# Kernel tuning notes

Hardware: AMD Instinct MI355X
Metric: run time of the kernel (lower is better)

## Reference

```python
import jax, jax.numpy as jnp
import numpy as np

N_NODES = 50000
N_EDGES = 800000
D_FEAT = 128


def setup_inputs() -> dict:
    key = jax.random.key(0)
    k1, k2, k3, k4, k5, k6 = jax.random.split(key, 6)
    input = jax.random.normal(k1, (N_NODES, D_FEAT), dtype=jnp.float32)
    h0 = jax.random.normal(k2, (N_NODES, D_FEAT), dtype=jnp.float32)
    # edge list + weights represent the sparse normalized adjacency used by torch.spmm
    edge_row = jax.random.randint(k3, (N_EDGES,), 0, N_NODES, dtype=jnp.int32)
    edge_col = jax.random.randint(k4, (N_EDGES,), 0, N_NODES, dtype=jnp.int32)
    edge_weight = jax.random.uniform(k5, (N_EDGES,), dtype=jnp.float32)
    # learned parameter: uniform(-stdv, stdv) with stdv = 1/sqrt(out_features)
    stdv = 1.0 / np.sqrt(D_FEAT)
    weight = jax.random.uniform(k6, (D_FEAT, D_FEAT), dtype=jnp.float32,
                                minval=-stdv, maxval=stdv)
    return {
        "input": input,
        "h0": h0,
        "weight": weight,
        "edge_row": edge_row,
        "edge_col": edge_col,
        "edge_weight": edge_weight,
        "lamda": jnp.float32(0.5),
        "alpha": jnp.float32(0.1),
        "l": 4,
    }


def reference(input, h0, weight, edge_row, edge_col, edge_weight, lamda, alpha, l):
    n = input.shape[0]
    # theta = min(1, log(lamda / l + 1))
    theta = jnp.minimum(jnp.float32(1.0), jnp.log(lamda / l + 1.0))
    # hi = spmm(adj, input): gather source features, scale by edge weight, scatter-add to dest rows
    hi = jax.ops.segment_sum(edge_weight[:, None] * input[edge_col], edge_row,
                             num_segments=n)  # [N, D]
    support = (1.0 - alpha) * hi + alpha * h0
    output = theta * (support @ weight) + (1.0 - theta) * support
    return output + input
```

## Files before the change

### kernel.cpp

```cpp
#include <hip/hip_runtime.h>
#include <hip/hip_fp16.h>

#define D_FEAT 128

typedef _Float16 half8_t __attribute__((ext_vector_type(8)));
typedef float float4_t __attribute__((ext_vector_type(4)));

__device__ __forceinline__ float h16_to_f(unsigned short u) {
    union { unsigned short u; _Float16 f; } cv; cv.u = u; return (float)cv.f;
}
__device__ __forceinline__ unsigned short f_to_h16(float f) {
    union { unsigned short u; _Float16 f; } cv; cv.f = (_Float16)f; return cv.u;
}

__global__ __launch_bounds__(256) void prep_kernel(
    const float* __restrict__ input, unsigned* __restrict__ inph_u2,
    const float* __restrict__ W, __half* __restrict__ wt16,
    unsigned* __restrict__ sedge4_slack,
    const int* __restrict__ erow, int* __restrict__ bucket_cnt,
    int nconv4, int n_edges, int convBlocks, int wBlocks)
{
    __shared__ int lh[256];
    const int bid = blockIdx.x;
    const int t = threadIdx.x;

    if (bid < convBlocks) {
        int tid = bid * 256 + t;
        if (tid < nconv4) {
            float4 v = reinterpret_cast<const float4*>(input)[tid];
            __half2 a = __floats2half2_rn(v.x, v.y);
            __half2 b = __floats2half2_rn(v.z, v.w);
            uint2 p;
            p.x = *reinterpret_cast<unsigned*>(&a);
            p.y = *reinterpret_cast<unsigned*>(&b);
            reinterpret_cast<uint2*>(inph_u2)[tid] = p;
        }
    } else if (bid < convBlocks + wBlocks) {
        int idx = (bid - convBlocks) * 256 + t;
        if (idx < D_FEAT * D_FEAT) {
            int n = idx >> 7, k = idx & 127;
            wt16[n * D_FEAT + k] = __float2half(W[k * D_FEAT + n]);
        }
    } else if (bid == convBlocks + wBlocks) {
        if (t < 16) sedge4_slack[t] = 0u;
    } else {
        int hb = bid - convBlocks - wBlocks - 1;
        lh[t] = 0;
        __syncthreads();
        int base = hb * 4096;
        int end = base + 4096; if (end > n_edges) end = n_edges;
        for (int i = base + t; i < end; i += 256)
            atomicAdd(&lh[erow[i] >> 8], 1);
        __syncthreads();
        int c = lh[t];
        if (c > 0) atomicAdd(&bucket_cnt[t], c);
    }
}

__global__ __launch_bounds__(256) void bucket_scan_kernel(
    const int* __restrict__ bucket_cnt, int* __restrict__ bcursor,
    int* __restrict__ bbase, int nb, int n_edges)
{
    __shared__ int lds[256];
    int t = threadIdx.x;
    int v = (t < nb) ? bucket_cnt[t] : 0;
    lds[t] = v;
    __syncthreads();
#pragma unroll
    for (int off = 1; off < 256; off <<= 1) {
        int add = (t >= off) ? lds[t - off] : 0;
        __syncthreads();
        lds[t] += add;
        __syncthreads();
    }
    if (t < nb) {
        int ex = lds[t] - v;
        bcursor[t] = ex;
        bbase[t] = ex;
    }
    if (t == 0) bbase[nb] = n_edges;
}

__global__ __launch_bounds__(256) void bin_kernel(
    const int* __restrict__ erow, const int* __restrict__ ecol,
    const float* __restrict__ ew, int* __restrict__ bcursor,
    uint2* __restrict__ btmp, int n_edges)
{
    __shared__ int lcnt[256];
    const int t = threadIdx.x;
    const int base = blockIdx.x * 4096;
    lcnt[t] = 0;
    __syncthreads();

    unsigned rc[16];
    float    wv[16];
#pragma unroll
    for (int i = 0; i < 16; ++i) {
        int idx = base + i * 256 + t;
        if (idx < n_edges) {
            int r = erow[idx];
            rc[i] = ((unsigned)r << 16) | (unsigned)ecol[idx];
            wv[i] = ew[idx];
            atomicAdd(&lcnt[r >> 8], 1);
        } else {
            rc[i] = 0xFFFFFFFFu;
        }
    }
    __syncthreads();
    int c = lcnt[t];
    int gbase = (c > 0) ? atomicAdd(&bcursor[t], c) : 0;
    lcnt[t] = gbase;
    __syncthreads();
#pragma unroll
    for (int i = 0; i < 16; ++i) {
        if (rc[i] != 0xFFFFFFFFu) {
            int b = rc[i] >> 24;
            int pos = atomicAdd(&lcnt[b], 1);
            uint2 p;
            p.x = rc[i];
            p.y = __float_as_uint(wv[i]);
            btmp[pos] = p;
        }
    }
}

__global__ __launch_bounds__(256) void sort_kernel(
    const uint2* __restrict__ btmp, const int* __restrict__ bbase,
    int* __restrict__ cnt, int* __restrict__ beg,
    unsigned* __restrict__ sedge4, int n)
{
    __shared__ int lscan[256];
    __shared__ int lofs[256];
    const int b = blockIdx.x;
    const int t = threadIdx.x;
    const int lo = bbase[b];
    const int hi = bbase[b + 1];

    lscan[t] = 0;
    __syncthreads();
    for (int i = lo + t; i < hi; i += 256) {
        int rl = (btmp[i].x >> 16) & 255;
        atomicAdd(&lscan[rl], 1);
    }
    __syncthreads();
    int v = lscan[t];
    __syncthreads();
#pragma unroll
    for (int off = 1; off < 256; off <<= 1) {
        int add = (t >= off) ? lscan[t - off] : 0;
        __syncthreads();
        lscan[t] += add;
        __syncthreads();
    }
    int ex = lscan[t] - v;
    lofs[t] = ex;
    int row = b * 256 + t;
    if (row < n) {
        cnt[row] = v;
        beg[row] = lo + ex;
    }
    __syncthreads();
    for (int i = lo + t; i < hi; i += 256) {
        uint2 p = btmp[i];
        int rl = (p.x >> 16) & 255;
        int pos = atomicAdd(&lofs[rl], 1);
        float w = __uint_as_float(p.y);
        sedge4[lo + pos] = (p.x & 0xFFFFu) | ((unsigned)f_to_h16(w) << 16);
    }
}

__global__ __launch_bounds__(256) void spmm4_kernel(
    const __half2* __restrict__ inph, const float* __restrict__ h0,
    const int* __restrict__ begp, const int* __restrict__ cnt,
    const unsigned* __restrict__ sedge4,
    const float* __restrict__ alpha_p, __half2* __restrict__ s16out, int n)
{
    int lane = threadIdx.x & 63;
    int row  = blockIdx.x * 4 + (threadIdx.x >> 6);
    if (row >= n) return;

    int deg = cnt[row];
    int beg = begp[row];

    float2 a0 = {0.f, 0.f}, a1 = {0.f, 0.f}, a2 = {0.f, 0.f}, a3 = {0.f, 0.f};
    for (int e = 0; e < deg; e += 16) {
        unsigned r[16];
#pragma unroll
        for (int i = 0; i < 16; ++i) r[i] = sedge4[beg + e + i];
        __half2 v[16];
#pragma unroll
        for (int i = 0; i < 16; ++i)
            v[i] = inph[(size_t)(r[i] & 0xFFFFu) * 64 + lane];
#pragma unroll
        for (int i = 0; i < 16; ++i) {
            float w = h16_to_f((e + i < deg) ? (unsigned short)(r[i] >> 16)
                                             : (unsigned short)0);
            float2 f = __half22float2(v[i]);
            if ((i & 3) == 0) { a0.x = fmaf(w, f.x, a0.x); a0.y = fmaf(w, f.y, a0.y); }
            if ((i & 3) == 1) { a1.x = fmaf(w, f.x, a1.x); a1.y = fmaf(w, f.y, a1.y); }
            if ((i & 3) == 2) { a2.x = fmaf(w, f.x, a2.x); a2.y = fmaf(w, f.y, a2.y); }
            if ((i & 3) == 3) { a3.x = fmaf(w, f.x, a3.x); a3.y = fmaf(w, f.y, a3.y); }
        }
    }
    float2 acc;
    acc.x = (a0.x + a1.x) + (a2.x + a3.x);
    acc.y = (a0.y + a1.y) + (a2.y + a3.y);

    const float alpha = alpha_p[0];
    const float oma   = 1.0f - alpha;
    float2 h = reinterpret_cast<const float2*>(h0)[(size_t)row * 64 + lane];
    float sx = fmaf(oma, acc.x, alpha * h.x);
    float sy = fmaf(oma, acc.y, alpha * h.y);
    s16out[(size_t)row * 64 + lane] = __floats2half2_rn(sx, sy);
}

__global__ __launch_bounds__(256) void gemm_mfma_kernel(
    const __half* __restrict__ s16, const __half* __restrict__ wt16,
    const float* __restrict__ input, float* __restrict__ out,
    const float* __restrict__ lamda_p, const int* __restrict__ l_p,
    int n_rows)
{
    const int wave = threadIdx.x >> 6;
    const int lane = threadIdx.x & 63;
    const int row0 = (blockIdx.x * 4 + wave) * 16;
    if (row0 >= n_rows) return;

    const int mr = lane & 15;
    const int kg = lane >> 4;

    const _Float16* sp = reinterpret_cast<const _Float16*>(s16);
    const _Float16* wp = reinterpret_cast<const _Float16*>(wt16);

    float4_t acc[8];
#pragma unroll
    for (int nt = 0; nt < 8; ++nt) acc[nt] = (float4_t){0.f, 0.f, 0.f, 0.f};

#pragma unroll
    for (int ks = 0; ks < 4; ++ks) {
        const int kofs = ks * 32 + kg * 8;
        half8_t a = *reinterpret_cast<const half8_t*>(
            sp + (size_t)(row0 + mr) * D_FEAT + kofs);
#pragma unroll
        for (int nt = 0; nt < 8; ++nt) {
            half8_t b = *reinterpret_cast<const half8_t*>(
                wp + (size_t)(nt * 16 + mr) * D_FEAT + kofs);
            acc[nt] = __builtin_amdgcn_mfma_f32_16x16x32_f16(a, b, acc[nt], 0, 0, 0);
        }
    }

    const float lamda = lamda_p[0];
    const float theta = fminf(1.0f, logf(lamda / (float)l_p[0] + 1.0f));
    const float om_theta = 1.0f - theta;

#pragma unroll
    for (int nt = 0; nt < 8; ++nt) {
#pragma unroll
        for (int r = 0; r < 4; ++r) {
            const int row = row0 + kg * 4 + r;
            const int col = nt * 16 + mr;
            const size_t idx = (size_t)row * D_FEAT + col;
            const float s = (float)sp[idx];
            out[idx] = fmaf(theta, acc[nt][r], fmaf(om_theta, s, input[idx]));
        }
    }
}

__global__ __launch_bounds__(256) void hist_kernel(
    const int* __restrict__ erow, int* __restrict__ cnt, int n_edges)
{
    int e = blockIdx.x * 256 + threadIdx.x;
    if (e < n_edges) atomicAdd(&cnt[erow[e]], 1);
}

__global__ __launch_bounds__(256) void prep_noW_kernel(
    const float* __restrict__ input, unsigned* __restrict__ inph_u2,
    const int* __restrict__ erow, int* __restrict__ cnt,
    int nconv4, int n_edges)
{
    int tid = blockIdx.x * 256 + threadIdx.x;
    if (tid < nconv4) {
        float4 v = reinterpret_cast<const float4*>(input)[tid];
        __half2 a = __floats2half2_rn(v.x, v.y);
        __half2 b = __floats2half2_rn(v.z, v.w);
        uint2 p;
        p.x = *reinterpret_cast<unsigned*>(&a);
        p.y = *reinterpret_cast<unsigned*>(&b);
        reinterpret_cast<uint2*>(inph_u2)[tid] = p;
    } else {
        int e = tid - nconv4;
        if (e < n_edges) atomicAdd(&cnt[erow[e]], 1);
    }
}

__global__ __launch_bounds__(256) void partial_kernel(
    const int* __restrict__ cnt, int* __restrict__ partial, int n)
{
    __shared__ int lds[4];
    int i = blockIdx.x * 256 + threadIdx.x;
    int v = (i < n) ? cnt[i] : 0;
#pragma unroll
    for (int off = 32; off > 0; off >>= 1) v += __shfl_down(v, off, 64);
    if ((threadIdx.x & 63) == 0) lds[threadIdx.x >> 6] = v;
    __syncthreads();
    if (threadIdx.x == 0)
        partial[blockIdx.x] = lds[0] + lds[1] + lds[2] + lds[3];
}

__global__ __launch_bounds__(256) void scan_partial_kernel(
    int* __restrict__ partial, int nb)
{
    __shared__ int lds[256];
    int t = threadIdx.x;
    int v = (t < nb) ? partial[t] : 0;
    lds[t] = v;
    __syncthreads();
#pragma unroll
    for (int off = 1; off < 256; off <<= 1) {
        int add = (t >= off) ? lds[t - off] : 0;
        __syncthreads();
        lds[t] += add;
        __syncthreads();
    }
    if (t < nb) partial[t] = lds[t] - v;
}

__global__ __launch_bounds__(256) void scan_final_kernel(
    const int* __restrict__ cnt, const int* __restrict__ partial,
    int* __restrict__ cursor, int n)
{
    __shared__ int lds[256];
    int t = threadIdx.x;
    int i = blockIdx.x * 256 + t;
    int v = (i < n) ? cnt[i] : 0;
    lds[t] = v;
    __syncthreads();
#pragma unroll
    for (int off = 1; off < 256; off <<= 1) {
        int add = (t >= off) ? lds[t - off] : 0;
        __syncthreads();
        lds[t] += add;
        __syncthreads();
    }
    if (i < n) cursor[i] = lds[t] - v + partial[blockIdx.x];
}

__global__ __launch_bounds__(256) void edge_scatter_kernel(
    const int* __restrict__ erow, const int* __restrict__ ecol,
    const float* __restrict__ ew, int* __restrict__ cursor,
    uint2* __restrict__ sedge, int n_edges)
{
    int e = blockIdx.x * 256 + threadIdx.x;
    if (e >= n_edges) return;
    int r = erow[e];
    int pos = atomicAdd(&cursor[r], 1);
    uint2 p;
    p.x = (unsigned)ecol[e];
    p.y = __float_as_uint(ew[e]);
    sedge[pos] = p;
}

__global__ __launch_bounds__(256) void spmm_fp16_kernel(
    const __half2* __restrict__ inph, const float* __restrict__ h0,
    const int* __restrict__ cursor, const int* __restrict__ cnt,
    const uint2* __restrict__ sedge,
    const float* __restrict__ alpha_p, float* __restrict__ outp, int n)
{
    int lane = threadIdx.x & 63;
    int row  = blockIdx.x * 4 + (threadIdx.x >> 6);
    if (row >= n) return;
    int deg = cnt[row];
    int beg = cursor[row] - deg;
    float2 accA = make_float2(0.f, 0.f), accB = make_float2(0.f, 0.f);
    int e = 0;
    for (; e + 2 <= deg; e += 2) {
        uint2 e0 = sedge[beg + e], e1 = sedge[beg + e + 1];
        __half2 v0 = inph[(size_t)e0.x * 64 + lane];
        __half2 v1 = inph[(size_t)e1.x * 64 + lane];
        float w0 = __uint_as_float(e0.y), w1 = __uint_as_float(e1.y);
        float2 f0 = __half22float2(v0), f1 = __half22float2(v1);
        accA.x = fmaf(w0, f0.x, accA.x); accA.y = fmaf(w0, f0.y, accA.y);
        accB.x = fmaf(w1, f1.x, accB.x); accB.y = fmaf(w1, f1.y, accB.y);
    }
    if (e < deg) {
        uint2 e0 = sedge[beg + e];
        __half2 v0 = inph[(size_t)e0.x * 64 + lane];
        float w0 = __uint_as_float(e0.y);
        float2 f0 = __half22float2(v0);
        accA.x = fmaf(w0, f0.x, accA.x); accA.y = fmaf(w0, f0.y, accA.y);
    }
    float2 acc; acc.x = accA.x + accB.x; acc.y = accA.y + accB.y;
    const float alpha = alpha_p[0], oma = 1.0f - alpha;
    float2 h = reinterpret_cast<const float2*>(h0)[(size_t)row * 64 + lane];
    float2 s;
    s.x = fmaf(oma, acc.x, alpha * h.x);
    s.y = fmaf(oma, acc.y, alpha * h.y);
    reinterpret_cast<float2*>(outp)[(size_t)row * 64 + lane] = s;
}

__global__ __launch_bounds__(256) void spmm_fp32_kernel(
    const float* __restrict__ input, const float* __restrict__ h0,
    const int* __restrict__ cursor, const int* __restrict__ cnt,
    const uint2* __restrict__ sedge,
    const float* __restrict__ alpha_p, float* __restrict__ outp, int n)
{
    int lane = threadIdx.x & 63;
    int row  = blockIdx.x * 4 + (threadIdx.x >> 6);
    if (row >= n) return;
    int deg = cnt[row];
    int beg = cursor[row] - deg;
    const float2* in2 = reinterpret_cast<const float2*>(input);
    float2 acc = make_float2(0.f, 0.f);
    for (int e = 0; e < deg; ++e) {
        uint2 ed = sedge[beg + e];
        float w = __uint_as_float(ed.y);
        float2 v = in2[(size_t)ed.x * 64 + lane];
        acc.x = fmaf(w, v.x, acc.x);
        acc.y = fmaf(w, v.y, acc.y);
    }
    const float alpha = alpha_p[0], oma = 1.0f - alpha;
    float2 h = reinterpret_cast<const float2*>(h0)[(size_t)row * 64 + lane];
    float2 s;
    s.x = fmaf(oma, acc.x, alpha * h.x);
    s.y = fmaf(oma, acc.y, alpha * h.y);
    reinterpret_cast<float2*>(outp)[(size_t)row * 64 + lane] = s;
}

__global__ __launch_bounds__(256) void fused_kernel(
    float* __restrict__ io, const float* __restrict__ input,
    const float* __restrict__ W,
    const float* __restrict__ lamda_p, const int* __restrict__ l_p,
    int n_rows)
{
    __shared__ float s_lds[2][D_FEAT];
    const int j = threadIdx.x & 127;
    const int r = threadIdx.x >> 7;
    float wcol[D_FEAT];
#pragma unroll
    for (int k = 0; k < D_FEAT; ++k) wcol[k] = W[k * D_FEAT + j];
    const float lamda = lamda_p[0];
    const float theta = fminf(1.0f, logf(lamda / (float)l_p[0] + 1.0f));
    const float om_theta = 1.0f - theta;
    for (int row0 = blockIdx.x * 2; row0 < n_rows; row0 += gridDim.x * 2) {
        const int row = row0 + r;
        const bool active = row < n_rows;
        float sj = 0.0f;
        if (active) {
            sj = io[(size_t)row * D_FEAT + j];
            s_lds[r][j] = sj;
        }
        __syncthreads();
        if (active) {
            float dot = 0.0f;
            const float4* s4 = reinterpret_cast<const float4*>(s_lds[r]);
#pragma unroll
            for (int k4 = 0; k4 < D_FEAT / 4; ++k4) {
                const float4 sv = s4[k4];
                dot = fmaf(sv.x, wcol[4 * k4 + 0], dot);
                dot = fmaf(sv.y, wcol[4 * k4 + 1], dot);
                dot = fmaf(sv.z, wcol[4 * k4 + 2], dot);
                dot = fmaf(sv.w, wcol[4 * k4 + 3], dot);
            }
            const size_t base = (size_t)row * D_FEAT + j;
            io[base] = fmaf(theta, dot, om_theta * sj) + input[base];
        }
        __syncthreads();
    }
}

extern "C" void kernel_launch(void* const* d_in, const int* in_sizes, int n_in,
                              void* d_out, int out_size, void* d_ws, size_t ws_size,
                              hipStream_t stream)
{
    const float* input = (const float*)d_in[0];
    const float* h0    = (const float*)d_in[1];
    const float* W     = (const float*)d_in[2];
    const int*   erow  = (const int*)d_in[3];
    const int*   ecol  = (const int*)d_in[4];
    const float* ew    = (const float*)d_in[5];
    const float* lamda = (const float*)d_in[6];
    const float* alpha = (const float*)d_in[7];
    const int*   l_p   = (const int*)d_in[8];
    float* out = (float*)d_out;

    const int n_nodes = in_sizes[0] / D_FEAT;
    const int n_edges = in_sizes[3];
    const int nb = (n_nodes + 255) / 256;
    const int nconv4 = n_nodes * D_FEAT / 4;
    const int histBlocks = (n_edges + 4095) / 4096;

    char* p = (char*)d_ws;
    auto align16 = [](char* q) {
        return (char*)(((uintptr_t)q + 15) & ~(uintptr_t)15);
    };
    int* cnt      = (int*)p;                    p += (size_t)n_nodes * 4;
    int* beg      = (int*)p;                    p += (size_t)n_nodes * 4;
    int* bucket_cnt = (int*)p;                  p += 256 * 4;
    int* bcursor  = (int*)p;                    p += 257 * 4;
    int* bbase    = (int*)p;                    p += 257 * 4;
    p = align16(p);
    unsigned* sedge4 = (unsigned*)p;            p += ((size_t)n_edges + 16) * 4;
    p = align16(p);
    unsigned* inph  = (unsigned*)p;             p += (size_t)n_nodes * D_FEAT * 2;
    p = align16(p);
    char* unionp = p;
    uint2*  btmp = (uint2*)unionp;
    __half* s16  = (__half*)unionp;
    size_t union_bytes = (size_t)n_nodes * D_FEAT * 2;
    if ((size_t)n_edges * 8 > union_bytes) union_bytes = (size_t)n_edges * 8;
    p += union_bytes;
    p = align16(p);
    __half* wt16 = (__half*)p;                  p += (size_t)D_FEAT * D_FEAT * 2;
    const size_t need_new = (size_t)(p - (char*)d_ws);

    const bool use_new = (ws_size >= need_new) && (n_nodes < 65536) && (nb <= 256);

    if (use_new) {
        const int convBlocks = (nconv4 + 255) / 256;
        const int wBlocks = (D_FEAT * D_FEAT + 255) / 256;
        const int totalBlocks = convBlocks + wBlocks + 1 + histBlocks;

        hipMemsetAsync(bucket_cnt, 0, 256 * sizeof(int), stream);
        prep_kernel<<<totalBlocks, 256, 0, stream>>>(
            input, inph, W, wt16, sedge4 + n_edges, erow, bucket_cnt,
            nconv4, n_edges, convBlocks, wBlocks);
        bucket_scan_kernel<<<1, 256, 0, stream>>>(
            bucket_cnt, bcursor, bbase, nb, n_edges);
        bin_kernel<<<histBlocks, 256, 0, stream>>>(
            erow, ecol, ew, bcursor, btmp, n_edges);
        sort_kernel<<<nb, 256, 0, stream>>>(
            btmp, bbase, cnt, beg, sedge4, n_nodes);
        spmm4_kernel<<<(n_nodes + 3) / 4, 256, 0, stream>>>(
            (const __half2*)inph, h0, beg, cnt, sedge4, alpha,
            (__half2*)s16, n_nodes);
        const int ntiles = (n_nodes + 15) / 16;
        gemm_mfma_kernel<<<(ntiles + 3) / 4, 256, 0, stream>>>(
            s16, wt16, input, out, lamda, l_p, n_nodes);
        return;
    }

    int*   fcnt     = (int*)d_ws;
    int*   fcursor  = fcnt + n_nodes;
    int*   fpartial = fcursor + n_nodes;
    uint2* fsedge   = (uint2*)(fpartial + 256);
    unsigned* finph = (unsigned*)(fsedge + n_edges);

    const size_t need_base = (size_t)(2 * n_nodes + 256) * 4 + (size_t)n_edges * 8;
    const size_t need_fp16 = need_base + (size_t)n_nodes * D_FEAT * 2;
    const bool use_fp16 = ws_size >= need_fp16;

    hipMemsetAsync(fcnt, 0, (size_t)n_nodes * sizeof(int), stream);

    if (use_fp16) {
        int total = nconv4 + n_edges;
        prep_noW_kernel<<<(total + 255) / 256, 256, 0, stream>>>(
            input, finph, erow, fcnt, nconv4, n_edges);
    } else {
        hist_kernel<<<(n_edges + 255) / 256, 256, 0, stream>>>(erow, fcnt, n_edges);
    }
    partial_kernel<<<nb, 256, 0, stream>>>(fcnt, fpartial, n_nodes);
    scan_partial_kernel<<<1, 256, 0, stream>>>(fpartial, nb);
    scan_final_kernel<<<nb, 256, 0, stream>>>(fcnt, fpartial, fcursor, n_nodes);
    edge_scatter_kernel<<<(n_edges + 255) / 256, 256, 0, stream>>>(
        erow, ecol, ew, fcursor, fsedge, n_edges);
    if (use_fp16) {
        spmm_fp16_kernel<<<(n_nodes + 3) / 4, 256, 0, stream>>>(
            (const __half2*)finph, h0, fcursor, fcnt, fsedge, alpha, out, n_nodes);
    } else {
        spmm_fp32_kernel<<<(n_nodes + 3) / 4, 256, 0, stream>>>(
            input, h0, fcursor, fcnt, fsedge, alpha, out, n_nodes);
    }
    fused_kernel<<<2048, 256, 0, stream>>>(out, input, W, lamda, l_p, n_nodes);
}
```

Baseline: 118.1 us.

## Fuse bucket scan into prep via last-block ticket; split SpMM wave into half-waves

The separate single-block bucket scan kernel is removed. Its work now runs inside prep_kernel, in whichever histogram block is the last to finish, detected with a global done counter and a threadfence, which saves one kernel launch. The SpMM kernel is reorganised so each half-wave handles alternate edges and loads 8-byte chunks (4 halves) per lane, with a cross-half shuffle reduction at the end. This halves the gathers issued per lane per 16-edge chunk and widens each load, at the cost of a final shuffle and an idle half-wave during the epilogue store.

```diff
diff --git a/kernel.cpp b/kernel.cpp
--- a/kernel.cpp
+++ b/kernel.cpp
@@ -18,9 +18,13 @@
     const float* __restrict__ W, __half* __restrict__ wt16,
     unsigned* __restrict__ sedge4_slack,
     const int* __restrict__ erow, int* __restrict__ bucket_cnt,
-    int nconv4, int n_edges, int convBlocks, int wBlocks)
+    int* __restrict__ done_ctr, int* __restrict__ bcursor,
+    int* __restrict__ bbase,
+    int nconv4, int n_edges, int convBlocks, int wBlocks,
+    int histBlocks, int nb)
 {
     __shared__ int lh[256];
+    __shared__ int ticket_s;
     const int bid = blockIdx.x;
     const int t = threadIdx.x;
 
@@ -54,31 +58,29 @@
         __syncthreads();
         int c = lh[t];
         if (c > 0) atomicAdd(&bucket_cnt[t], c);
-    }
-}
-
-__global__ __launch_bounds__(256) void bucket_scan_kernel(
-    const int* __restrict__ bucket_cnt, int* __restrict__ bcursor,
-    int* __restrict__ bbase, int nb, int n_edges)
-{
-    __shared__ int lds[256];
-    int t = threadIdx.x;
-    int v = (t < nb) ? bucket_cnt[t] : 0;
-    lds[t] = v;
-    __syncthreads();
-#pragma unroll
-    for (int off = 1; off < 256; off <<= 1) {
-        int add = (t >= off) ? lds[t - off] : 0;
-        __syncthreads();
-        lds[t] += add;
-        __syncthreads();
-    }
-    if (t < nb) {
-        int ex = lds[t] - v;
-        bcursor[t] = ex;
-        bbase[t] = ex;
-    }
-    if (t == 0) bbase[nb] = n_edges;
+        __threadfence();
+        __syncthreads();
+        if (t == 0) ticket_s = atomicAdd(done_ctr, 1);
+        __syncthreads();
+        if (ticket_s == histBlocks - 1) {
+            int v = (t < nb) ? atomicAdd(&bucket_cnt[t], 0) : 0;
+            lh[t] = v;
+            __syncthreads();
+#pragma unroll
+            for (int off = 1; off < 256; off <<= 1) {
+                int add = (t >= off) ? lh[t - off] : 0;
+                __syncthreads();
+                lh[t] += add;
+                __syncthreads();
+            }
+            if (t < nb) {
+                int ex = lh[t] - v;
+                bcursor[t] = ex;
+                bbase[t] = ex;
+            }
+            if (t == 0) bbase[nb] = n_edges;
+        }
+    }
 }
 
 __global__ __launch_bounds__(256) void bin_kernel(
@@ -170,48 +172,90 @@
 }
 
 __global__ __launch_bounds__(256) void spmm4_kernel(
-    const __half2* __restrict__ inph, const float* __restrict__ h0,
+    const uint2* __restrict__ inph2, const float* __restrict__ h0,
     const int* __restrict__ begp, const int* __restrict__ cnt,
     const unsigned* __restrict__ sedge4,
-    const float* __restrict__ alpha_p, __half2* __restrict__ s16out, int n)
-{
-    int lane = threadIdx.x & 63;
-    int row  = blockIdx.x * 4 + (threadIdx.x >> 6);
+    const float* __restrict__ alpha_p, uint2* __restrict__ s16out, int n)
+{
+    const int lane = threadIdx.x & 63;
+    const int row  = blockIdx.x * 4 + (threadIdx.x >> 6);
     if (row >= n) return;
 
-    int deg = cnt[row];
-    int beg = begp[row];
-
-    float2 a0 = {0.f, 0.f}, a1 = {0.f, 0.f}, a2 = {0.f, 0.f}, a3 = {0.f, 0.f};
+    const int g  = lane >> 5;
+    const int fl = lane & 31;
+
+    const int deg = cnt[row];
+    const int beg = begp[row];
+
+    float4 accA = {0.f, 0.f, 0.f, 0.f};
+    float4 accB = {0.f, 0.f, 0.f, 0.f};
+
     for (int e = 0; e < deg; e += 16) {
-        unsigned r[16];
-#pragma unroll
-        for (int i = 0; i < 16; ++i) r[i] = sedge4[beg + e + i];
-        __half2 v[16];
-#pragma unroll
-        for (int i = 0; i < 16; ++i)
-            v[i] = inph[(size_t)(r[i] & 0xFFFFu) * 64 + lane];
-#pragma unroll
-        for (int i = 0; i < 16; ++i) {
-            float w = h16_to_f((e + i < deg) ? (unsigned short)(r[i] >> 16)
-                                             : (unsigned short)0);
-            float2 f = __half22float2(v[i]);
-            if ((i & 3) == 0) { a0.x = fmaf(w, f.x, a0.x); a0.y = fmaf(w, f.y, a0.y); }
-            if ((i & 3) == 1) { a1.x = fmaf(w, f.x, a1.x); a1.y = fmaf(w, f.y, a1.y); }
-            if ((i & 3) == 2) { a2.x = fmaf(w, f.x, a2.x); a2.y = fmaf(w, f.y, a2.y); }
-            if ((i & 3) == 3) { a3.x = fmaf(w, f.x, a3.x); a3.y = fmaf(w, f.y, a3.y); }
-        }
-    }
-    float2 acc;
-    acc.x = (a0.x + a1.x) + (a2.x + a3.x);
-    acc.y = (a0.y + a1.y) + (a2.y + a3.y);
-
-    const float alpha = alpha_p[0];
-    const float oma   = 1.0f - alpha;
-    float2 h = reinterpret_cast<const float2*>(h0)[(size_t)row * 64 + lane];
-    float sx = fmaf(oma, acc.x, alpha * h.x);
-    float sy = fmaf(oma, acc.y, alpha * h.y);
-    s16out[(size_t)row * 64 + lane] = __floats2half2_rn(sx, sy);
+        unsigned r0 = sedge4[beg + e +  0 + g];
+        unsigned r1 = sedge4[beg + e +  2 + g];
+        unsigned r2 = sedge4[beg + e +  4 + g];
+        unsigned r3 = sedge4[beg + e +  6 + g];
+        unsigned r4 = sedge4[beg + e +  8 + g];
+        unsigned r5 = sedge4[beg + e + 10 + g];
+        unsigned r6 = sedge4[beg + e + 12 + g];
+        unsigned r7 = sedge4[beg + e + 14 + g];
+        uint2 v0 = inph2[(size_t)(r0 & 0xFFFFu) * 32 + fl];
+        uint2 v1 = inph2[(size_t)(r1 & 0xFFFFu) * 32 + fl];
+        uint2 v2 = inph2[(size_t)(r2 & 0xFFFFu) * 32 + fl];
+        uint2 v3 = inph2[(size_t)(r3 & 0xFFFFu) * 32 + fl];
+        uint2 v4 = inph2[(size_t)(r4 & 0xFFFFu) * 32 + fl];
+        uint2 v5 = inph2[(size_t)(r5 & 0xFFFFu) * 32 + fl];
+        uint2 v6 = inph2[(size_t)(r6 & 0xFFFFu) * 32 + fl];
+        uint2 v7 = inph2[(size_t)(r7 & 0xFFFFu) * 32 + fl];
+        float w0 = h16_to_f((e +  0 + g < deg) ? (unsigned short)(r0 >> 16) : (unsigned short)0);
+        float w1 = h16_to_f((e +  2 + g < deg) ? (unsigned short)(r1 >> 16) : (unsigned short)0);
+        float w2 = h16_to_f((e +  4 + g < deg) ? (unsigned short)(r2 >> 16) : (unsigned short)0);
+        float w3 = h16_to_f((e +  6 + g < deg) ? (unsigned short)(r3 >> 16) : (unsigned short)0);
+        float w4 = h16_to_f((e +  8 + g < deg) ? (unsigned short)(r4 >> 16) : (unsigned short)0);
+        float w5 = h16_to_f((e + 10 + g < deg) ? (unsigned short)(r5 >> 16) : (unsigned short)0);
+        float w6 = h16_to_f((e + 12 + g < deg) ? (unsigned short)(r6 >> 16) : (unsigned short)0);
+        float w7 = h16_to_f((e + 14 + g < deg) ? (unsigned short)(r7 >> 16) : (unsigned short)0);
+        float2 f01, f23;
+#define ACCUM(vv, ww, AC)                                                      \
+        f01 = __half22float2(*reinterpret_cast<const __half2*>(&(vv).x));      \
+        f23 = __half22float2(*reinterpret_cast<const __half2*>(&(vv).y));      \
+        AC.x = fmaf(ww, f01.x, AC.x); AC.y = fmaf(ww, f01.y, AC.y);            \
+        AC.z = fmaf(ww, f23.x, AC.z); AC.w = fmaf(ww, f23.y, AC.w);
+        ACCUM(v0, w0, accA)
+        ACCUM(v1, w1, accB)
+        ACCUM(v2, w2, accA)
+        ACCUM(v3, w3, accB)
+        ACCUM(v4, w4, accA)
+        ACCUM(v5, w5, accB)
+        ACCUM(v6, w6, accA)
+        ACCUM(v7, w7, accB)
+#undef ACCUM
+    }
+    float4 acc;
+    acc.x = accA.x + accB.x;
+    acc.y = accA.y + accB.y;
+    acc.z = accA.z + accB.z;
+    acc.w = accA.w + accB.w;
+    acc.x += __shfl_xor(acc.x, 32, 64);
+    acc.y += __shfl_xor(acc.y, 32, 64);
+    acc.z += __shfl_xor(acc.z, 32, 64);
+    acc.w += __shfl_xor(acc.w, 32, 64);
+
+    if (g == 0) {
+        const float alpha = alpha_p[0];
+        const float oma   = 1.0f - alpha;
+        float4 h = reinterpret_cast<const float4*>(h0)[(size_t)row * 32 + fl];
+        float s0 = fmaf(oma, acc.x, alpha * h.x);
+        float s1 = fmaf(oma, acc.y, alpha * h.y);
+        float s2 = fmaf(oma, acc.z, alpha * h.z);
+        float s3 = fmaf(oma, acc.w, alpha * h.w);
+        __half2 p0 = __floats2half2_rn(s0, s1);
+        __half2 p1 = __floats2half2_rn(s2, s3);
+        uint2 pk;
+        pk.x = *reinterpret_cast<unsigned*>(&p0);
+        pk.y = *reinterpret_cast<unsigned*>(&p1);
+        s16out[(size_t)row * 32 + fl] = pk;
+    }
 }
 
 __global__ __launch_bounds__(256) void gemm_mfma_kernel(
@@ -492,11 +536,12 @@
     auto align16 = [](char* q) {
         return (char*)(((uintptr_t)q + 15) & ~(uintptr_t)15);
     };
-    int* cnt      = (int*)p;                    p += (size_t)n_nodes * 4;
-    int* beg      = (int*)p;                    p += (size_t)n_nodes * 4;
+    int* cnt        = (int*)p;                  p += (size_t)n_nodes * 4;
+    int* beg        = (int*)p;                  p += (size_t)n_nodes * 4;
     int* bucket_cnt = (int*)p;                  p += 256 * 4;
-    int* bcursor  = (int*)p;                    p += 257 * 4;
-    int* bbase    = (int*)p;                    p += 257 * 4;
+    int* done_ctr   = (int*)p;                  p += 4;
+    int* bcursor    = (int*)p;                  p += 257 * 4;
+    int* bbase      = (int*)p;                  p += 257 * 4;
     p = align16(p);
     unsigned* sedge4 = (unsigned*)p;            p += ((size_t)n_edges + 16) * 4;
     p = align16(p);
@@ -519,19 +564,18 @@
         const int wBlocks = (D_FEAT * D_FEAT + 255) / 256;
         const int totalBlocks = convBlocks + wBlocks + 1 + histBlocks;
 
-        hipMemsetAsync(bucket_cnt, 0, 256 * sizeof(int), stream);
+        hipMemsetAsync(bucket_cnt, 0, 257 * sizeof(int), stream);
         prep_kernel<<<totalBlocks, 256, 0, stream>>>(
             input, inph, W, wt16, sedge4 + n_edges, erow, bucket_cnt,
-            nconv4, n_edges, convBlocks, wBlocks);
-        bucket_scan_kernel<<<1, 256, 0, stream>>>(
-            bucket_cnt, bcursor, bbase, nb, n_edges);
+            done_ctr, bcursor, bbase,
+            nconv4, n_edges, convBlocks, wBlocks, histBlocks, nb);
         bin_kernel<<<histBlocks, 256, 0, stream>>>(
             erow, ecol, ew, bcursor, btmp, n_edges);
         sort_kernel<<<nb, 256, 0, stream>>>(
             btmp, bbase, cnt, beg, sedge4, n_nodes);
         spmm4_kernel<<<(n_nodes + 3) / 4, 256, 0, stream>>>(
-            (const __half2*)inph, h0, beg, cnt, sedge4, alpha,
-            (__half2*)s16, n_nodes);
+            (const uint2*)inph, h0, beg, cnt, sedge4, alpha,
+            (uint2*)s16, n_nodes);
         const int ntiles = (n_nodes + 15) / 16;
         gemm_mfma_kernel<<<(ntiles + 3) / 4, 256, 0, stream>>>(
             s16, wt16, input, out, lamda, l_p, n_nodes);
```

After: 130.3 us. +10.3%, slower.

## Fuse CSR bucket scan, binning and sort into one grid-barrier kernel

Applied to the files above, without the earlier changes.

Replaces the bucket-scan, bin and sort kernels with a single kernel. Each block redundantly scans the bucket counts, bins its edges, then waits on a global atomic spin barrier before sorting its bucket. This removes two kernel launches and their inter-kernel gaps, at the risk of deadlock if not all blocks are co-resident. The GEMM epilogue also reads the residual input from the existing fp16 copy instead of fp32, halving that read traffic at some accuracy cost.

```diff
diff --git a/kernel.cpp b/kernel.cpp
--- a/kernel.cpp
+++ b/kernel.cpp
@@ -57,115 +57,122 @@
     }
 }
 
-__global__ __launch_bounds__(256) void bucket_scan_kernel(
-    const int* __restrict__ bucket_cnt, int* __restrict__ bcursor,
-    int* __restrict__ bbase, int nb, int n_edges)
-{
-    __shared__ int lds[256];
-    int t = threadIdx.x;
-    int v = (t < nb) ? bucket_cnt[t] : 0;
-    lds[t] = v;
-    __syncthreads();
-#pragma unroll
-    for (int off = 1; off < 256; off <<= 1) {
-        int add = (t >= off) ? lds[t - off] : 0;
-        __syncthreads();
-        lds[t] += add;
-        __syncthreads();
-    }
-    if (t < nb) {
-        int ex = lds[t] - v;
-        bcursor[t] = ex;
-        bbase[t] = ex;
-    }
-    if (t == 0) bbase[nb] = n_edges;
-}
-
-__global__ __launch_bounds__(256) void bin_kernel(
+__global__ __launch_bounds__(256) void coop_csr_kernel(
+    const int* __restrict__ bucket_cnt, int* __restrict__ reserve,
+    int* __restrict__ bar,
     const int* __restrict__ erow, const int* __restrict__ ecol,
-    const float* __restrict__ ew, int* __restrict__ bcursor,
-    uint2* __restrict__ btmp, int n_edges)
-{
+    const float* __restrict__ ew, uint2* __restrict__ btmp,
+    int* __restrict__ cnt, int* __restrict__ beg,
+    unsigned* __restrict__ sedge4,
+    int n_edges, int n, int histBlocks, int nb, int nblk)
+{
+    __shared__ int lbase[256];
     __shared__ int lcnt[256];
-    const int t = threadIdx.x;
-    const int base = blockIdx.x * 4096;
-    lcnt[t] = 0;
-    __syncthreads();
-
-    unsigned rc[16];
-    float    wv[16];
-#pragma unroll
-    for (int i = 0; i < 16; ++i) {
-        int idx = base + i * 256 + t;
-        if (idx < n_edges) {
-            int r = erow[idx];
-            rc[i] = ((unsigned)r << 16) | (unsigned)ecol[idx];
-            wv[i] = ew[idx];
-            atomicAdd(&lcnt[r >> 8], 1);
-        } else {
-            rc[i] = 0xFFFFFFFFu;
-        }
-    }
-    __syncthreads();
-    int c = lcnt[t];
-    int gbase = (c > 0) ? atomicAdd(&bcursor[t], c) : 0;
-    lcnt[t] = gbase;
-    __syncthreads();
-#pragma unroll
-    for (int i = 0; i < 16; ++i) {
-        if (rc[i] != 0xFFFFFFFFu) {
-            int b = rc[i] >> 24;
-            int pos = atomicAdd(&lcnt[b], 1);
-            uint2 p;
-            p.x = rc[i];
-            p.y = __float_as_uint(wv[i]);
-            btmp[pos] = p;
-        }
-    }
-}
-
-__global__ __launch_bounds__(256) void sort_kernel(
-    const uint2* __restrict__ btmp, const int* __restrict__ bbase,
-    int* __restrict__ cnt, int* __restrict__ beg,
-    unsigned* __restrict__ sedge4, int n)
-{
-    __shared__ int lscan[256];
     __shared__ int lofs[256];
     const int b = blockIdx.x;
     const int t = threadIdx.x;
-    const int lo = bbase[b];
-    const int hi = bbase[b + 1];
-
-    lscan[t] = 0;
-    __syncthreads();
-    for (int i = lo + t; i < hi; i += 256) {
-        int rl = (btmp[i].x >> 16) & 255;
-        atomicAdd(&lscan[rl], 1);
-    }
-    __syncthreads();
-    int v = lscan[t];
+
+    int bc = bucket_cnt[t];
+    lbase[t] = bc;
     __syncthreads();
 #pragma unroll
     for (int off = 1; off < 256; off <<= 1) {
-        int add = (t >= off) ? lscan[t - off] : 0;
-        __syncthreads();
-        lscan[t] += add;
-        __syncthreads();
-    }
-    int ex = lscan[t] - v;
-    lofs[t] = ex;
-    int row = b * 256 + t;
-    if (row < n) {
-        cnt[row] = v;
-        beg[row] = lo + ex;
-    }
-    __syncthreads();
-    for (int i = lo + t; i < hi; i += 256) {
-        uint2 p = btmp[i];
-        int rl = (p.x >> 16) & 255;
-        int pos = atomicAdd(&lofs[rl], 1);
-        float w = __uint_as_float(p.y);
-        sedge4[lo + pos] = (p.x & 0xFFFFu) | ((unsigned)f_to_h16(w) << 16);
+        int add = (t >= off) ? lbase[t - off] : 0;
+        __syncthreads();
+        lbase[t] += add;
+        __syncthreads();
+    }
+    {
+        int inc = lbase[t];
+        __syncthreads();
+        lbase[t] = inc - bc;
+    }
+    __syncthreads();
+
+    if (b < histBlocks) {
+        lcnt[t] = 0;
+        __syncthreads();
+        const int base = b * 4096;
+        unsigned rc[16];
+        float    wv[16];
+#pragma unroll
+        for (int i = 0; i < 16; ++i) {
+            int idx = base + i * 256 + t;
+            if (idx < n_edges) {
+                int r = erow[idx];
+                rc[i] = ((unsigned)r << 16) | (unsigned)ecol[idx];
+                wv[i] = ew[idx];
+                atomicAdd(&lcnt[r >> 8], 1);
+            } else {
+                rc[i] = 0xFFFFFFFFu;
+            }
+        }
+        __syncthreads();
+        int c = lcnt[t];
+        int gbase = 0;
+        if (c > 0) gbase = lbase[t] + atomicAdd(&reserve[t], c);
+        lcnt[t] = gbase;
+        __syncthreads();
+#pragma unroll
+        for (int i = 0; i < 16; ++i) {
+            if (rc[i] != 0xFFFFFFFFu) {
+                int bk = rc[i] >> 24;
+                int pos = atomicAdd(&lcnt[bk], 1);
+                uint2 p;
+                p.x = rc[i];
+                p.y = __float_as_uint(wv[i]);
+                btmp[pos] = p;
+            }
+        }
+    }
+
+    __syncthreads();
+    __threadfence();
+    if (t == 0) {
+        atomicAdd(bar, 1);
+        while (__hip_atomic_load(bar, __ATOMIC_RELAXED,
+                                 __HIP_MEMORY_SCOPE_AGENT) < nblk) {
+            __builtin_amdgcn_s_sleep(4);
+        }
+    }
+    __syncthreads();
+    __threadfence();
+
+    if (b < nb) {
+        const int lo = lbase[b];
+        const int hi = lo + bucket_cnt[b];
+
+        lcnt[t] = 0;
+        __syncthreads();
+        for (int i = lo + t; i < hi; i += 256) {
+            int rl = (btmp[i].x >> 16) & 255;
+            atomicAdd(&lcnt[rl], 1);
+        }
+        __syncthreads();
+        int v = lcnt[t];
+        __syncthreads();
+#pragma unroll
+        for (int off = 1; off < 256; off <<= 1) {
+            int add = (t >= off) ? lcnt[t - off] : 0;
+            __syncthreads();
+            lcnt[t] += add;
+            __syncthreads();
+        }
+        int ex = lcnt[t] - v;
+        lofs[t] = ex;
+        int row = b * 256 + t;
+        if (row < n) {
+            cnt[row] = v;
+            beg[row] = lo + ex;
+        }
+        __syncthreads();
+        for (int i = lo + t; i < hi; i += 256) {
+            uint2 p = btmp[i];
+            int rl = (p.x >> 16) & 255;
+            int pos = atomicAdd(&lofs[rl], 1);
+            float w = __uint_as_float(p.y);
+            sedge4[lo + pos] = (p.x & 0xFFFFu) | ((unsigned)f_to_h16(w) << 16);
+        }
     }
 }
 
@@ -216,7 +223,7 @@
 
 __global__ __launch_bounds__(256) void gemm_mfma_kernel(
     const __half* __restrict__ s16, const __half* __restrict__ wt16,
-    const float* __restrict__ input, float* __restrict__ out,
+    const __half* __restrict__ in16, float* __restrict__ out,
     const float* __restrict__ lamda_p, const int* __restrict__ l_p,
     int n_rows)
 {
@@ -230,6 +237,7 @@
 
     const _Float16* sp = reinterpret_cast<const _Float16*>(s16);
     const _Float16* wp = reinterpret_cast<const _Float16*>(wt16);
+    const _Float16* ip = reinterpret_cast<const _Float16*>(in16);
 
     float4_t acc[8];
 #pragma unroll
@@ -260,7 +268,7 @@
             const int col = nt * 16 + mr;
             const size_t idx = (size_t)row * D_FEAT + col;
             const float s = (float)sp[idx];
-            out[idx] = fmaf(theta, acc[nt][r], fmaf(om_theta, s, input[idx]));
+            out[idx] = fmaf(theta, acc[nt][r], fmaf(om_theta, s, (float)ip[idx]));
         }
     }
 }
@@ -492,11 +500,11 @@
     auto align16 = [](char* q) {
         return (char*)(((uintptr_t)q + 15) & ~(uintptr_t)15);
     };
-    int* cnt      = (int*)p;                    p += (size_t)n_nodes * 4;
-    int* beg      = (int*)p;                    p += (size_t)n_nodes * 4;
+    int* cnt        = (int*)p;                  p += (size_t)n_nodes * 4;
+    int* beg        = (int*)p;                  p += (size_t)n_nodes * 4;
     int* bucket_cnt = (int*)p;                  p += 256 * 4;
-    int* bcursor  = (int*)p;                    p += 257 * 4;
-    int* bbase    = (int*)p;                    p += 257 * 4;
+    int* reserve    = (int*)p;                  p += 256 * 4;
+    int* bar        = (int*)p;                  p += 4;
     p = align16(p);
     unsigned* sedge4 = (unsigned*)p;            p += ((size_t)n_edges + 16) * 4;
     p = align16(p);
@@ -512,29 +520,28 @@
     __half* wt16 = (__half*)p;                  p += (size_t)D_FEAT * D_FEAT * 2;
     const size_t need_new = (size_t)(p - (char*)d_ws);
 
-    const bool use_new = (ws_size >= need_new) && (n_nodes < 65536) && (nb <= 256);
+    const int coopBlocks = (histBlocks > nb) ? histBlocks : nb;
+    const bool use_new = (ws_size >= need_new) && (n_nodes < 65536) &&
+                         (nb <= 256) && (coopBlocks <= 256);
 
     if (use_new) {
         const int convBlocks = (nconv4 + 255) / 256;
         const int wBlocks = (D_FEAT * D_FEAT + 255) / 256;
         const int totalBlocks = convBlocks + wBlocks + 1 + histBlocks;
 
-        hipMemsetAsync(bucket_cnt, 0, 256 * sizeof(int), stream);
+        hipMemsetAsync(bucket_cnt, 0, 513 * sizeof(int), stream);
         prep_kernel<<<totalBlocks, 256, 0, stream>>>(
             input, inph, W, wt16, sedge4 + n_edges, erow, bucket_cnt,
             nconv4, n_edges, convBlocks, wBlocks);
-        bucket_scan_kernel<<<1, 256, 0, stream>>>(
-            bucket_cnt, bcursor, bbase, nb, n_edges);
-        bin_kernel<<<histBlocks, 256, 0, stream>>>(
-            erow, ecol, ew, bcursor, btmp, n_edges);
-        sort_kernel<<<nb, 256, 0, stream>>>(
-            btmp, bbase, cnt, beg, sedge4, n_nodes);
+        coop_csr_kernel<<<coopBlocks, 256, 0, stream>>>(
+            bucket_cnt, reserve, bar, erow, ecol, ew, btmp,
+            cnt, beg, sedge4, n_edges, n_nodes, histBlocks, nb, coopBlocks);
         spmm4_kernel<<<(n_nodes + 3) / 4, 256, 0, stream>>>(
             (const __half2*)inph, h0, beg, cnt, sedge4, alpha,
             (__half2*)s16, n_nodes);
         const int ntiles = (n_nodes + 15) / 16;
         gemm_mfma_kernel<<<(ntiles + 3) / 4, 256, 0, stream>>>(
-            s16, wt16, input, out, lamda, l_p, n_nodes);
+            s16, wt16, (const __half*)inph, out, lamda, l_p, n_nodes);
         return;
     }
 
```

After: 167.1 us. +41.4%, slower.
